# Performance work log

Hardware: AMD Instinct MI355X
Metric: run time of the kernel (lower is better)

## Reference

```python
import jax, jax.numpy as jnp
import numpy as np

B, T, N, H = 512, 128, 128, 256


def setup_inputs() -> dict:
    key = jax.random.key(0)
    ks = jax.random.split(key, 8)
    rn = lambda k, shape, sc: (jax.random.normal(k, shape, jnp.float32) * sc)
    return {
        "data": rn(ks[0], (B, T, N), 1.0),
        "h0": jnp.zeros((B, H), jnp.float32),
        # SimpleRNNCell params: h_t = tanh(x@Wx + h@Wh + b)
        "Wx": rn(ks[1], (N, H), 0.05),
        "Wh": rn(ks[2], (H, H), 0.05),
        "b": jnp.zeros((H,), jnp.float32),
        # InputAttention: w1: Dense(T) over last dim T; w2: Dense(T) over hidden; v: Dense(1)
        "W1": rn(ks[3], (T, T), 0.05),
        "b1": jnp.zeros((T,), jnp.float32),
        "W2": rn(ks[4], (H, T), 0.05),
        "b2": jnp.zeros((T,), jnp.float32),
        "Wv": rn(ks[5], (T, 1), 0.05),
        "bv": jnp.zeros((1,), jnp.float32),
        "n": N,
    }


def reference(data, h0, Wx, Wh, b, W1, b1, W2, b2, Wv, bv, n):
    # data: (B, T, n); h0: (B, H)
    Tlen = data.shape[1]
    x_perm = jnp.swapaxes(data, 1, 2)          # (B, n, T) == Permute((2,1))(x)
    pre = x_perm @ W1 + b1                      # w1(x_perm): loop-invariant, hoisted

    def step(h, x_t):
        # SimpleRNNCell: new state used for this step's attention
        h_new = jnp.tanh(x_t @ Wx + h @ Wh + b)                 # (B, H)
        q = h_new @ W2 + b2                                      # w2(RepeatVector(n)(h)) per row -> (B, T)
        score = jnp.tanh(pre + q[:, None, :])                    # (B, n, T)
        e = score @ Wv + bv                                      # (B, n, 1)
        e = jnp.swapaxes(e, 1, 2)                                # Permute((2,1)) -> (B, 1, n)
        alpha = jax.nn.softmax(e, axis=-1)                       # softmax over n
        return h_new, alpha

    xs = jnp.swapaxes(data, 0, 1)               # (T, B, n): data[:, t, :] per step
    _, alphas = jax.lax.scan(step, h0, xs)      # (T, B, 1, n)
    # faithful to tf.reshape(alpha_seq.stack(), (-1, T, n))
    alpha_seq = alphas.reshape(-1, Tlen, n)     # (B, T, n)
    return data * alpha_seq
```

## Files before the change

kernel.cpp:

```cpp
#include <hip/hip_runtime.h>


#define C2L 2.8853900817779268f
#define L2E 1.4426950408889634f

typedef _Float16 hf;
typedef _Float16 hf2 __attribute__((ext_vector_type(2)));
typedef _Float16 hf4 __attribute__((ext_vector_type(4)));
typedef _Float16 hf8 __attribute__((ext_vector_type(8)));
typedef float f32x4 __attribute__((ext_vector_type(4)));

__device__ __forceinline__ float fast_exp2(float x){
#if __has_builtin(__builtin_amdgcn_exp2f)
  return __builtin_amdgcn_exp2f(x);
#else
  return exp2f(x);
#endif
}
__device__ __forceinline__ float fast_rcp(float x){
#if __has_builtin(__builtin_amdgcn_rcpf)
  return __builtin_amdgcn_rcpf(x);
#else
  return 1.f/x;
#endif
}
__device__ __forceinline__ float dot2f(hf2 a, hf2 b, float c){
#if __has_builtin(__builtin_amdgcn_fdot2)
  return __builtin_amdgcn_fdot2(a, b, c, false);
#else
  return c + (float)a.x*(float)b.x + (float)a.y*(float)b.y;
#endif
}

__global__ __launch_bounds__(256) void k_prep_w(const float* __restrict__ Wx,
    const float* __restrict__ W2, const float* __restrict__ W1,
    hf* __restrict__ wts){
  int tid = blockIdx.x*256 + threadIdx.x;
  if (tid < 32768){
    int n = tid >> 7, k = tid & 127;
    wts[tid] = (hf)Wx[k*256 + n];
  } else if (tid < 65536){
    int t2 = tid - 32768;
    int n = t2 >> 8, k = t2 & 255;
    wts[tid] = (hf)W2[k*128 + n];
  } else {
    int t3 = tid - 65536;
    int n = t3 >> 7, k = t3 & 127;
    wts[tid] = (hf)W1[k*128 + n];
  }
}

template<int K, int MODE>
__global__ __launch_bounds__(256) void k_gemm(const void* __restrict__ Asrc,
    const hf* __restrict__ Bt, const float* __restrict__ bias,
    float* __restrict__ Cout){
  constexpr int SA = 136;
  __shared__ alignas(16) hf As[64*SA];
  __shared__ alignas(16) hf Bs[128*SA];
  const int tid = threadIdx.x;
  const int w = tid >> 6, lane = tid & 63;
  const int c = lane & 15, q = lane >> 4;
  const int bx = blockIdx.x;
  const int col0 = (MODE==0) ? blockIdx.y*128 : 0;

  float br[8];
  #pragma unroll
  for (int ni=0; ni<8; ni++) br[ni] = bias[col0 + ni*16 + c];

  f32x4 acc[8];
  #pragma unroll
  for (int ni=0; ni<8; ni++) acc[ni] = (f32x4){0.f,0.f,0.f,0.f};

  for (int kc=0; kc<K/128; kc++){
    if (MODE == 0){
      const float* A = (const float*)Asrc + (long)bx*64*128;
      #pragma unroll
      for (int v=0; v<8; v++){
        int f4 = v*256 + tid;
        int m = f4 >> 5, k4 = (f4 & 31)*4;
        float4 d = *(const float4*)&A[m*128 + k4];
        hf4 h = {(hf)d.x,(hf)d.y,(hf)d.z,(hf)d.w};
        *(hf4*)&As[m*SA + k4] = h;
      }
    } else if (MODE == 1){
      const hf* A = (const hf*)Asrc + (long)bx*64*256;
      #pragma unroll
      for (int v=0; v<4; v++){
        int f8 = v*256 + tid;
        int m = f8 >> 4, k8 = (f8 & 15)*8;
        *(hf8*)&As[m*SA + k8] = *(const hf8*)&A[m*256 + kc*128 + k8];
      }
    } else {
      const float* A = (const float*)Asrc + (long)(bx>>1)*16384;
      const int i0 = (bx & 1)*64;
      #pragma unroll
      for (int v=0; v<8; v++){
        int f4 = v*256 + tid;
        int t = f4 >> 4, i4 = (f4 & 15)*4;
        float4 d = *(const float4*)&A[t*128 + i0 + i4];
        As[(i4+0)*SA + t] = (hf)d.x;
        As[(i4+1)*SA + t] = (hf)d.y;
        As[(i4+2)*SA + t] = (hf)d.z;
        As[(i4+3)*SA + t] = (hf)d.w;
      }
    }
    #pragma unroll
    for (int v=0; v<8; v++){
      int f8 = v*256 + tid;
      int n = f8 >> 4, k8 = (f8 & 15)*8;
      *(hf8*)&Bs[n*SA + k8] = *(const hf8*)&Bt[(col0+n)*K + kc*128 + k8];
    }
    __syncthreads();
    #pragma unroll
    for (int kk=0; kk<4; kk++){
      hf8 a = *(const hf8*)&As[(w*16 + c)*SA + kk*32 + q*8];
      #pragma unroll
      for (int ni=0; ni<8; ni++){
        hf8 b = *(const hf8*)&Bs[(ni*16 + c)*SA + kk*32 + q*8];
        acc[ni] = __builtin_amdgcn_mfma_f32_16x16x32_f16(a, b, acc[ni], 0, 0, 0);
      }
    }
    __syncthreads();
  }
  #pragma unroll
  for (int ni=0; ni<8; ni++){
    #pragma unroll
    for (int r=0; r<4; r++){
      int rloc = w*16 + q*4 + r;
      int col = col0 + ni*16 + c;
      float val = acc[ni][r] + br[ni];
      int addr;
      if (MODE == 0){
        int R = bx*64 + rloc;
        int b_ = R >> 7, t_ = R & 127;
        addr = (t_*512 + b_)*256 + col;
      } else if (MODE == 1){
        int R = bx*64 + rloc;
        addr = R*128 + col;
        val = fast_exp2(C2L*val);
      } else {
        int b_ = bx >> 1, i_ = (bx & 1)*64 + rloc;
        addr = b_*16384 + i_*128 + col;
        val = fast_exp2(C2L*val);
      }
      Cout[addr] = val;
    }
  }
}

__global__ __launch_bounds__(256, 3) void k_rnn(const float* __restrict__ h0,
    const float* __restrict__ Wh, const float* __restrict__ xw,
    hf* __restrict__ Hb){
  __shared__ alignas(16) hf h_s[2][256];
  const int j = threadIdx.x;
  const int bb = blockIdx.x;
  hf2 wreg[128];
  #pragma unroll
  for (int m=0;m<128;m++){
    float w0 = Wh[(2*m)*256 + j];
    float w1 = Wh[(2*m+1)*256 + j];
    wreg[m] = (hf2){(hf)w0, (hf)w1};
  }
  h_s[0][j] = (hf)h0[bb*256 + j];
  float z = xw[(0*512 + bb)*256 + j];
  __syncthreads();
  for (int t=0;t<128;t++){
    int p = t & 1;
    float zn = (t < 127) ? xw[((t+1)*512 + bb)*256 + j] : 0.f;
    const hf8* h8 = (const hf8*)(&h_s[p][0]);
    float a[8];
    #pragma unroll
    for (int u=0;u<8;u++) a[u]=0.f;
    #pragma unroll
    for (int mm=0; mm<32; mm++){
      hf8 hv = h8[mm];
      hf2 h0p = {hv[0],hv[1]}, h1p = {hv[2],hv[3]};
      hf2 h2p = {hv[4],hv[5]}, h3p = {hv[6],hv[7]};
      a[(4*mm+0)&7] = dot2f(wreg[4*mm+0], h0p, a[(4*mm+0)&7]);
      a[(4*mm+1)&7] = dot2f(wreg[4*mm+1], h1p, a[(4*mm+1)&7]);
      a[(4*mm+2)&7] = dot2f(wreg[4*mm+2], h2p, a[(4*mm+2)&7]);
      a[(4*mm+3)&7] = dot2f(wreg[4*mm+3], h3p, a[(4*mm+3)&7]);
    }
    float v = z + (((a[0]+a[1])+(a[2]+a[3])) + ((a[4]+a[5])+(a[6]+a[7])));
    float e2 = fast_exp2(v*C2L);
    float hn = 1.f - 2.f*fast_rcp(e2 + 1.f);
    Hb[(t*512+bb)*256 + j] = (hf)hn;
    h_s[p^1][j] = (hf)hn;
    z = zn;
    __syncthreads();
  }
}

__global__ __launch_bounds__(256, 4) void k_attn(const float* __restrict__ P,
    const float* __restrict__ Qm, const float* __restrict__ Wv,
    const float* __restrict__ data, float* __restrict__ out){
  __shared__ alignas(16) float qs[32*128];
  __shared__ alignas(16) float wvs[128];
  __shared__ alignas(16) float epart[2][2][4][128];
  __shared__ float red[2][4][2];
  const int b = blockIdx.x, tile = blockIdx.y;
  const int tid = threadIdx.x;
  const int i = tid & 127, hl = tid >> 7;
  const int t0 = tile*32;
  if (tid < 128) wvs[tid] = -2.f*Wv[tid];
  #pragma unroll
  for (int v=0; v<4; v++){
    int flat = v*1024 + tid*4;
    int tt = flat >> 7, c = flat & 127;
    *(float4*)&qs[flat] = *(const float4*)&Qm[((t0+tt)*512 + b)*128 + c];
  }
  float4 p4[16];
  const float* prow = P + b*16384 + i*128 + hl*64;
  #pragma unroll
  for (int v=0; v<16; v++) p4[v] = *(const float4*)&prow[v*4];
  __syncthreads();
  for (int tp=0; tp<8; tp++){
    const int pp = tp & 1;
    const float* q0r = &qs[(4*tp)*128   + hl*64];
    const float* q1r = &qs[(4*tp+1)*128 + hl*64];
    const float* q2r = &qs[(4*tp+2)*128 + hl*64];
    const float* q3r = &qs[(4*tp+3)*128 + hl*64];
    const float* wvr = &wvs[hl*64];
    float acc0=0.f, acc1=0.f, acc2=0.f, acc3=0.f;
    #pragma unroll
    for (int m=0; m<16; m++){
      float4 Pv = p4[m];
      float4 wv = *(const float4*)&wvr[m*4];
      {
        float4 qq = *(const float4*)&q0r[m*4];
        float u = fmaf(Pv.x, qq.x, 1.f), v = fmaf(Pv.y, qq.y, 1.f);
        float n = fmaf(wv.x, v, wv.y*u);
        acc0 = fmaf(n, fast_rcp(u*v), acc0);
        float u2 = fmaf(Pv.z, qq.z, 1.f), v2 = fmaf(Pv.w, qq.w, 1.f);
        float n2 = fmaf(wv.z, v2, wv.w*u2);
        acc0 = fmaf(n2, fast_rcp(u2*v2), acc0);
      }
      {
        float4 qq = *(const float4*)&q1r[m*4];
        float u = fmaf(Pv.x, qq.x, 1.f), v = fmaf(Pv.y, qq.y, 1.f);
        float n = fmaf(wv.x, v, wv.y*u);
        acc1 = fmaf(n, fast_rcp(u*v), acc1);
        float u2 = fmaf(Pv.z, qq.z, 1.f), v2 = fmaf(Pv.w, qq.w, 1.f);
        float n2 = fmaf(wv.z, v2, wv.w*u2);
        acc1 = fmaf(n2, fast_rcp(u2*v2), acc1);
      }
      {
        float4 qq = *(const float4*)&q2r[m*4];
        float u = fmaf(Pv.x, qq.x, 1.f), v = fmaf(Pv.y, qq.y, 1.f);
        float n = fmaf(wv.x, v, wv.y*u);
        acc2 = fmaf(n, fast_rcp(u*v), acc2);
        float u2 = fmaf(Pv.z, qq.z, 1.f), v2 = fmaf(Pv.w, qq.w, 1.f);
        float n2 = fmaf(wv.z, v2, wv.w*u2);
        acc2 = fmaf(n2, fast_rcp(u2*v2), acc2);
      }
      {
        float4 qq = *(const float4*)&q3r[m*4];
        float u = fmaf(Pv.x, qq.x, 1.f), v = fmaf(Pv.y, qq.y, 1.f);
        float n = fmaf(wv.x, v, wv.y*u);
        acc3 = fmaf(n, fast_rcp(u*v), acc3);
        float u2 = fmaf(Pv.z, qq.z, 1.f), v2 = fmaf(Pv.w, qq.w, 1.f);
        float n2 = fmaf(wv.z, v2, wv.w*u2);
        acc3 = fmaf(n2, fast_rcp(u2*v2), acc3);
      }
    }
    epart[pp][hl][0][i] = acc0;
    epart[pp][hl][1][i] = acc1;
    epart[pp][hl][2][i] = acc2;
    epart[pp][hl][3][i] = acc3;
    __syncthreads();
    const int g = tid >> 7;
    float pe[2];
    #pragma unroll
    for (int s=0; s<2; s++){
      int tl = g + 2*s;
      float e = epart[pp][0][tl][i] + epart[pp][1][tl][i];
      pe[s] = fast_exp2(e*L2E);
      float sm = pe[s];
      #pragma unroll
      for (int off=32; off; off>>=1) sm += __shfl_xor(sm, off);
      if ((tid & 63) == 0) red[pp][tl][(tid>>6)&1] = sm;
    }
    __syncthreads();
    #pragma unroll
    for (int s=0; s<2; s++){
      int tl = g + 2*s;
      float ssum = red[pp][tl][0] + red[pp][tl][1];
      float alpha = pe[s] * fast_rcp(ssum);
      int t = t0 + 4*tp + tl;
      int base = (t*512 + b)*128 + i;
      out[base] = data[base]*alpha;
    }
  }
}

extern "C" void kernel_launch(void* const* d_in, const int* in_sizes, int n_in,
                              void* d_out, int out_size, void* d_ws, size_t ws_size,
                              hipStream_t stream) {
  const float* data = (const float*)d_in[0];
  const float* h0   = (const float*)d_in[1];
  const float* Wx   = (const float*)d_in[2];
  const float* Wh   = (const float*)d_in[3];
  const float* bb   = (const float*)d_in[4];
  const float* W1   = (const float*)d_in[5];
  const float* b1   = (const float*)d_in[6];
  const float* W2   = (const float*)d_in[7];
  const float* b2   = (const float*)d_in[8];
  const float* Wv   = (const float*)d_in[9];
  float* wsp = (float*)d_ws;
  float* P   = wsp;
  float* xwQ = wsp + 8388608;
  hf*    Hbf = (hf*)(wsp + 25165824);
  hf*    wts = (hf*)(wsp + 33554432);
  const hf* Wxt = wts;
  const hf* W2t = wts + 32768;
  const hf* W1t = wts + 65536;
  float* out = (float*)d_out;

  hipLaunchKernelGGL(k_prep_w, dim3(320), dim3(256), 0, stream, Wx, W2, W1, wts);
  hipLaunchKernelGGL((k_gemm<128,0>), dim3(1024,2), dim3(256), 0, stream,
                     (const void*)data, Wxt, bb, xwQ);
  hipLaunchKernelGGL((k_gemm<128,2>), dim3(1024),   dim3(256), 0, stream,
                     (const void*)data, W1t, b1, P);
  hipLaunchKernelGGL(k_rnn, dim3(512), dim3(256), 0, stream, h0, Wh, xwQ, Hbf);
  hipLaunchKernelGGL((k_gemm<256,1>), dim3(1024),   dim3(256), 0, stream,
                     (const void*)Hbf, W2t, b2, xwQ);
  hipLaunchKernelGGL(k_attn, dim3(512, 4), dim3(256), 0, stream, P, xwQ, Wv, data, out);
}
```

Baseline: 392.5 us.

## Rewrite RNN recurrence as MFMA matmul over 16-row batch tiles

The recurrent step previously used one block per batch row, with each thread computing one hidden unit through scalar fdot2 against register-held Wh columns. It now uses 32 blocks of 512 threads, each handling 16 batch rows. Each step is a 16x256x256 matmul on MFMA 16x16x32 f16 instructions, with h held in an XOR-swizzled LDS layout and Wh fragments kept in registers. This moves the sequential part onto matrix cores and amortizes Wh across 16 rows, at the cost of running only 32 workgroups on a large GPU.

```diff
diff --git a/kernel.cpp b/kernel.cpp
--- a/kernel.cpp
+++ b/kernel.cpp
@@ -22,13 +22,6 @@
   return __builtin_amdgcn_rcpf(x);
 #else
   return 1.f/x;
-#endif
-}
-__device__ __forceinline__ float dot2f(hf2 a, hf2 b, float c){
-#if __has_builtin(__builtin_amdgcn_fdot2)
-  return __builtin_amdgcn_fdot2(a, b, c, false);
-#else
-  return c + (float)a.x*(float)b.x + (float)a.y*(float)b.y;
 #endif
 }
 
@@ -148,45 +141,88 @@
   }
 }
 
-__global__ __launch_bounds__(256, 3) void k_rnn(const float* __restrict__ h0,
+__global__ __launch_bounds__(512, 2) void k_rnn(const float* __restrict__ h0,
     const float* __restrict__ Wh, const float* __restrict__ xw,
     hf* __restrict__ Hb){
-  __shared__ alignas(16) hf h_s[2][256];
-  const int j = threadIdx.x;
-  const int bb = blockIdx.x;
-  hf2 wreg[128];
-  #pragma unroll
-  for (int m=0;m<128;m++){
-    float w0 = Wh[(2*m)*256 + j];
-    float w1 = Wh[(2*m+1)*256 + j];
-    wreg[m] = (hf2){(hf)w0, (hf)w1};
-  }
-  h_s[0][j] = (hf)h0[bb*256 + j];
-  float z = xw[(0*512 + bb)*256 + j];
+  __shared__ alignas(16) char hs[2*8192];
+  const int tid = threadIdx.x;
+  const int w = tid >> 6, lane = tid & 63;
+  const int c = lane & 15, q = lane >> 4;
+  const int b0 = blockIdx.x * 16;
+  const int w0 = w * 32;
+  hf8 bw[2][8];
+  #pragma unroll
+  for (int nt=0; nt<2; nt++){
+    #pragma unroll
+    for (int kc=0; kc<8; kc++){
+      #pragma unroll
+      for (int e=0; e<8; e++){
+        bw[nt][kc][e] = (hf)Wh[(kc*32 + q*8 + e)*256 + w0 + nt*16 + c];
+      }
+    }
+  }
+  {
+    int m = tid >> 5, s8 = tid & 31;
+    const float* src = &h0[(b0 + m)*256 + s8*8];
+    float4 d0 = *(const float4*)&src[0];
+    float4 d1 = *(const float4*)&src[4];
+    hf8 hv = {(hf)d0.x,(hf)d0.y,(hf)d0.z,(hf)d0.w,
+              (hf)d1.x,(hf)d1.y,(hf)d1.z,(hf)d1.w};
+    *(hf8*)&hs[m*512 + ((s8 ^ (m & 7)) << 4)] = hv;
+  }
+  float xwv[2][4];
+  #pragma unroll
+  for (int nt=0; nt<2; nt++){
+    #pragma unroll
+    for (int r=0; r<4; r++)
+      xwv[nt][r] = xw[(b0 + q*4 + r)*256 + w0 + nt*16 + c];
+  }
   __syncthreads();
-  for (int t=0;t<128;t++){
-    int p = t & 1;
-    float zn = (t < 127) ? xw[((t+1)*512 + bb)*256 + j] : 0.f;
-    const hf8* h8 = (const hf8*)(&h_s[p][0]);
-    float a[8];
-    #pragma unroll
-    for (int u=0;u<8;u++) a[u]=0.f;
-    #pragma unroll
-    for (int mm=0; mm<32; mm++){
-      hf8 hv = h8[mm];
-      hf2 h0p = {hv[0],hv[1]}, h1p = {hv[2],hv[3]};
-      hf2 h2p = {hv[4],hv[5]}, h3p = {hv[6],hv[7]};
-      a[(4*mm+0)&7] = dot2f(wreg[4*mm+0], h0p, a[(4*mm+0)&7]);
-      a[(4*mm+1)&7] = dot2f(wreg[4*mm+1], h1p, a[(4*mm+1)&7]);
-      a[(4*mm+2)&7] = dot2f(wreg[4*mm+2], h2p, a[(4*mm+2)&7]);
-      a[(4*mm+3)&7] = dot2f(wreg[4*mm+3], h3p, a[(4*mm+3)&7]);
-    }
-    float v = z + (((a[0]+a[1])+(a[2]+a[3])) + ((a[4]+a[5])+(a[6]+a[7])));
-    float e2 = fast_exp2(v*C2L);
-    float hn = 1.f - 2.f*fast_rcp(e2 + 1.f);
-    Hb[(t*512+bb)*256 + j] = (hf)hn;
-    h_s[p^1][j] = (hf)hn;
-    z = zn;
+  const int m = c;
+  const int abase = m*512;
+  for (int t=0; t<128; t++){
+    const int p = t & 1;
+    float xwn[2][4];
+    if (t < 127){
+      #pragma unroll
+      for (int nt=0; nt<2; nt++){
+        #pragma unroll
+        for (int r=0; r<4; r++)
+          xwn[nt][r] = xw[((t+1)*512 + b0 + q*4 + r)*256 + w0 + nt*16 + c];
+      }
+    } else {
+      #pragma unroll
+      for (int nt=0; nt<2; nt++){
+        #pragma unroll
+        for (int r=0; r<4; r++) xwn[nt][r] = 0.f;
+      }
+    }
+    hf8 a[8];
+    #pragma unroll
+    for (int kc=0; kc<8; kc++)
+      a[kc] = *(const hf8*)&hs[p*8192 + abase + ((((kc<<2)|q) ^ (m & 7)) << 4)];
+    f32x4 acc0 = (f32x4){0.f,0.f,0.f,0.f};
+    f32x4 acc1 = (f32x4){0.f,0.f,0.f,0.f};
+    #pragma unroll
+    for (int kc=0; kc<8; kc++){
+      acc0 = __builtin_amdgcn_mfma_f32_16x16x32_f16(a[kc], bw[0][kc], acc0, 0,0,0);
+      acc1 = __builtin_amdgcn_mfma_f32_16x16x32_f16(a[kc], bw[1][kc], acc1, 0,0,0);
+    }
+    #pragma unroll
+    for (int nt=0; nt<2; nt++){
+      #pragma unroll
+      for (int r=0; r<4; r++){
+        float v = (nt ? acc1[r] : acc0[r]) + xwv[nt][r];
+        float e2 = fast_exp2(v*C2L);
+        float hn = 1.f - 2.f*fast_rcp(e2 + 1.f);
+        int row = q*4 + r;
+        int col = w0 + nt*16 + c;
+        *(hf*)&hs[(p^1)*8192 + row*512
+                  + (((col >> 3) ^ (row & 7)) << 4) + (col & 7)*2] = (hf)hn;
+        Hb[(t*512 + b0 + row)*256 + col] = (hf)hn;
+        xwv[nt][r] = xwn[nt][r];
+      }
+    }
     __syncthreads();
   }
 }
@@ -321,7 +357,7 @@
                      (const void*)data, Wxt, bb, xwQ);
   hipLaunchKernelGGL((k_gemm<128,2>), dim3(1024),   dim3(256), 0, stream,
                      (const void*)data, W1t, b1, P);
-  hipLaunchKernelGGL(k_rnn, dim3(512), dim3(256), 0, stream, h0, Wh, xwQ, Hbf);
+  hipLaunchKernelGGL(k_rnn, dim3(32), dim3(512), 0, stream, h0, Wh, xwQ, Hbf);
   hipLaunchKernelGGL((k_gemm<256,1>), dim3(1024),   dim3(256), 0, stream,
                      (const void*)Hbf, W2t, b2, xwQ);
   hipLaunchKernelGGL(k_attn, dim3(512, 4), dim3(256), 0, stream, P, xwQ, Wv, data, out);
```

New measurement: 372.7 us. 1.05x faster.
